# Optimization experiments

Measured on AMD Instinct MI355X. Metric: run time of the kernel, lower is better.

The kernel has to match this reference:

```python
import jax, jax.numpy as jnp
import numpy as np
import math

B, T = 16, 512
P = 256          # num_memory_positions
E = 128          # embedding_dim
NB = 4           # num_beings
K = 4            # attention_radius
TEMP = 8.0       # attention_temperature
PHI = 1.618033988749895


def setup_inputs() -> dict:
    key = jax.random.key(0)
    ks = jax.random.split(key, 8)
    x = jax.random.normal(ks[0], (B, T, 8), jnp.float32)
    W_in = jax.random.normal(ks[1], (8, E), jnp.float32) * 0.1
    b_in = jnp.zeros((E,), jnp.float32)
    W_out = jax.random.normal(ks[2], (E, 8), jnp.float32) * 0.1
    b_out = jnp.zeros((8,), jnp.float32)
    W_p = jax.random.normal(ks[3], (E, E), jnp.float32) * (1.0 / np.sqrt(E))
    b_p = jnp.zeros((E,), jnp.float32)
    ptr_dest = jax.random.uniform(ks[4], (NB, P), jnp.float32) * P
    jump_W = jax.random.normal(ks[5], (NB, E), jnp.float32) * 0.1
    jump_b = jnp.zeros((NB,), jnp.float32)
    ctx_strength = jnp.full((NB,), 0.2, jnp.float32)
    pe = np.zeros((NB, E), np.float32)
    for i in range(NB):
        ph = i * PHI
        v = []
        for h in range(1, 9):
            v += [math.sin(h * ph), math.cos(h * ph)]
        pe[i, :16] = v  # phase_embedding padded with zeros to E (E >= 16)
    phase_bias = jnp.asarray(pe)
    seg = P / NB
    pointer_init = jax.random.uniform(ks[6], (NB, B), jnp.float32) * seg + jnp.arange(NB, dtype=jnp.float32)[:, None] * seg
    return dict(x=x, W_in=W_in, b_in=b_in, W_out=W_out, b_out=b_out,
                W_p=W_p, b_p=b_p, ptr_dest=ptr_dest, jump_W=jump_W,
                jump_b=jump_b, ctx_strength=ctx_strength,
                phase_bias=phase_bias, pointer_init=pointer_init)


def _forward(x, W_in, b_in, W_out, b_out, W_p, b_p, ptr_dest, jump_W,
             jump_b, ctx_strength, phase_bias, pointer_init):
    offsets = jnp.arange(-K, K + 1)          # [W]
    b_ix = jnp.arange(B)                     # [B]
    half = P / 2.0
    ring0 = jnp.zeros((B, P, E), x.dtype)
    hid0 = jnp.zeros((NB, B, E), x.dtype)

    def step(carry, x_t):
        ring, ptrs, hids = carry
        inp = x_t @ W_in + b_in              # [B,E]
        outs, new_ptrs, new_hids = [], [], []
        for i in range(NB):                  # beings sequential (share ring)
            ptr, hid = ptrs[i], hids[i]
            base = jnp.clip(jnp.floor(ptr).astype(jnp.int32), 0, P - 1)
            idx = (base[:, None] + offsets[None, :]) % P            # [B,W]
            delta = jnp.mod(idx.astype(x_t.dtype) - ptr[:, None] + half, P) - half
            w = jax.nn.softmax(-(delta ** 2) / TEMP, axis=1)         # [B,W]
            nbhd = ring[b_ix[:, None], idx]                          # [B,W,E]
            ctx = jnp.sum(w[..., None] * nbhd, axis=1)               # [B,E]
            comb = inp + jax.nn.sigmoid(ctx_strength[i]) * ctx + 0.1 * phase_bias[i]
            s = jnp.tanh(comb + hid)
            s = jnp.tanh(s @ W_p + b_p)      # depth-1 = 1 processing layer
            ring = ring.at[b_ix[:, None], idx].add(w[..., None] * s[:, None, :])
            cur = jnp.clip(ptr.astype(jnp.int32), 0, P - 1)
            jump_target = ptr_dest[i][cur]                           # [B]
            probs = jax.nn.sigmoid(s @ jump_W[i] + jump_b[i])        # [B]
            hard = (probs > 0.5).astype(s.dtype)
            should_jump = hard - jax.lax.stop_gradient(probs) + probs
            walk = (ptr + 1.0) % P
            new_ptrs.append(jnp.where(should_jump > 0.5, jump_target, walk))
            new_hids.append(s)
            outs.append(s @ W_out + b_out)                           # [B,8]
        out_t = jnp.mean(jnp.stack(outs), axis=0)                    # [B,8] (training-mode mean)
        return (ring, jnp.stack(new_ptrs), jnp.stack(new_hids)), out_t

    _, ys = jax.lax.scan(step, (ring0, pointer_init, hid0), jnp.swapaxes(x, 0, 1))
    return jnp.swapaxes(ys, 0, 1)            # [B,T,8]


def reference(x, W_in, b_in, W_out, b_out, W_p, b_p, ptr_dest, jump_W,
              jump_b, ctx_strength, phase_bias, pointer_init):
    return _forward(x, W_in, b_in, W_out, b_out, W_p, b_p, ptr_dest,
                    jump_W, jump_b, ctx_strength, phase_bias, pointer_init)
```

## Files before the change

kernel.cpp:

```cpp
#include <hip/hip_runtime.h>
#include <cmath>

namespace {
constexpr int B_ = 16, T_ = 512, P_ = 256, E_ = 128, NB_ = 4, K_ = 4;
constexpr int THREADS_ = 512;
constexpr int RS_ = 132;

__device__ __forceinline__ float rcpf(float x) { return __builtin_amdgcn_rcpf(x); }
__device__ __forceinline__ float fast_tanh(float x) {
    float a = fabsf(x);
    float t = __expf(-2.0f * a);
    float r = 1.0f - 2.0f * t * rcpf(1.0f + t);
    return copysignf(r, x);
}

__device__ __forceinline__ void lgkm_barrier() {
    __builtin_amdgcn_sched_barrier(0);
    asm volatile("s_waitcnt lgkmcnt(0)\n\ts_barrier" ::: "memory");
    __builtin_amdgcn_sched_barrier(0);
}

template<int CTRL>
__device__ __forceinline__ float dpp_addf(float v) {
    const int s = __builtin_amdgcn_update_dpp(0, __float_as_int(v), CTRL, 0xF, 0xF, true);
    return v + __int_as_float(s);
}
template<int Q>
__device__ __forceinline__ float dpp_bcast4(float v) {
    const int s = __builtin_amdgcn_update_dpp(0, __float_as_int(v), Q * 0x55, 0xF, 0xF, true);
    return __int_as_float(s);
}
template<int Q>
__device__ __forceinline__ int dpp_bcast4i(int v) {
    return __builtin_amdgcn_update_dpp(0, v, Q * 0x55, 0xF, 0xF, true);
}
__device__ __forceinline__ float pl16_sum(float v) {
#if __has_builtin(__builtin_amdgcn_permlane16_swap)
    const unsigned u = __float_as_uint(v);
    const auto r = __builtin_amdgcn_permlane16_swap(u, u, false, false);
    return __uint_as_float(r[0]) + __uint_as_float(r[1]);
#else
    return v + __shfl_xor(v, 16);
#endif
}
__device__ __forceinline__ float pl32_sum(float v) {
#if __has_builtin(__builtin_amdgcn_permlane32_swap)
    const unsigned u = __float_as_uint(v);
    const auto r = __builtin_amdgcn_permlane32_swap(u, u, false, false);
    return __uint_as_float(r[0]) + __uint_as_float(r[1]);
#else
    return v + __shfl_xor(v, 32);
#endif
}
__device__ __forceinline__ float redkq8(float v) {
    v = dpp_addf<0x128>(v);
    v = pl16_sum(v);
    v = pl32_sum(v);
    return v;
}
__device__ __forceinline__ float redpair(float v) {
    v = dpp_addf<0xB1>(v);
    v = dpp_addf<0x4E>(v);
    v = dpp_addf<0x141>(v);
    return v;
}
__device__ __forceinline__ float sel4(int q, float a, float b, float c, float d) {
    const float t0 = (q & 1) ? b : a;
    const float t1 = (q & 1) ? d : c;
    return (q & 2) ? t1 : t0;
}
__device__ __forceinline__ float sel8f(int kq, float w0, float w1, float w2, float w3,
                                       float w4, float w5, float w6, float w7) {
    const float a = (kq & 1) ? w1 : w0;
    const float b = (kq & 1) ? w3 : w2;
    const float c = (kq & 1) ? w5 : w4;
    const float d = (kq & 1) ? w7 : w6;
    const float e = (kq & 2) ? b : a;
    const float f = (kq & 2) ? d : c;
    return (kq & 4) ? f : e;
}
}

__global__ __launch_bounds__(512, 1)
void swarm_ring_kernel(const float* __restrict__ x,
                       const float* __restrict__ W_in,
                       const float* __restrict__ b_in,
                       const float* __restrict__ W_out,
                       const float* __restrict__ b_out,
                       const float* __restrict__ W_p,
                       const float* __restrict__ b_p,
                       const float* __restrict__ ptr_dest,
                       const float* __restrict__ jump_W,
                       const float* __restrict__ jump_b,
                       const float* __restrict__ ctx_strength,
                       const float* __restrict__ phase_bias,
                       const float* __restrict__ pointer_init,
                       float* __restrict__ out)
{
    __shared__ alignas(16) float  ring[P_ * RS_];
    __shared__ alignas(16) float4 s4[136];
    __shared__ alignas(16) float  sbuf[2][160];
    __shared__ alignas(16) float  red[32];
    __shared__ alignas(16) float  hist[16][132];
    __shared__ alignas(16) float  wout_s[8][132];

    const int tid = threadIdx.x;
    const int b   = blockIdx.x;
    const int w   = tid >> 6;
    const int l   = tid & 63;
    const int s_  = l & 7;
    const int kq  = l >> 3;
    const int e0  = ((w << 3) | s_) << 1;
    const int bq  = l & 3;

    for (int k4 = tid; k4 < P_ * RS_ / 4; k4 += THREADS_)
        ((float4*)ring)[k4] = make_float4(0.f, 0.f, 0.f, 0.f);
    for (int idx = tid; idx < 8 * E_; idx += THREADS_) {
        const int m = idx >> 7, ee = idx & 127;
        wout_s[m][ee] = W_out[ee * 8 + m] * 0.25f;
    }

    float2 wp2[16];
    #pragma unroll
    for (int kk = 0; kk < 16; ++kk)
        wp2[kk] = *(const float2*)(W_p + (kq * 16 + kk) * E_ + e0);

    float2 wi2[8];
    #pragma unroll
    for (int k = 0; k < 8; ++k)
        wi2[k] = *(const float2*)(W_in + k * E_ + e0);

    const float2 bin2 = *(const float2*)(b_in + e0);
    const float2 bp2  = *(const float2*)(b_p + e0);
    const float  bout_m = b_out[tid & 7];

    float2 pb2[NB_], jw2[NB_], hid2[NB_];
    float  sigc[NB_], jb_r[NB_], ptrv[NB_];
    #pragma unroll
    for (int i = 0; i < NB_; ++i) {
        const float2 pb = *(const float2*)(phase_bias + i * E_ + e0);
        pb2[i] = make_float2(0.1f * pb.x, 0.1f * pb.y);
        jw2[i] = *(const float2*)(jump_W + i * E_ + e0);
        sigc[i] = 1.0f / (1.0f + __expf(-ctx_strength[i]));
        jb_r[i] = jump_b[i];
        hid2[i] = make_float2(0.f, 0.f);
        ptrv[i] = pointer_init[i * B_ + b];
    }

    const float* xb = x + (size_t)b * T_ * 8;
    float xt[8];
    {
        float4 a0 = ((const float4*)xb)[0], a1 = ((const float4*)xb)[1];
        xt[0]=a0.x; xt[1]=a0.y; xt[2]=a0.z; xt[3]=a0.w;
        xt[4]=a1.x; xt[5]=a1.y; xt[6]=a1.z; xt[7]=a1.w;
    }

    const float Cw1 = 0.8824969f, Cw2 = 0.60653066f, Cw3 = 0.32465247f, Cw4 = 0.13533528f;
    const float Dw1 = 0.7788008f, Dw2 = 0.36787944f, Dw3 = 0.105399225f, Dw4 = 0.018315639f;

    __syncthreads();

    for (int t = 0; t < T_; ++t) {
        const float p_own    = sel4(bq, ptrv[0], ptrv[1], ptrv[2], ptrv[3]);
        const int   base_own = (int)p_own;
        const float jt_own   = ptr_dest[(bq << 8) + base_own];
        const float f_own    = p_own - (float)base_own;
        float wsel_own, w8_own, psinv_own;
        {
            const float r  = __expf(0.25f * f_own);
            const float r2 = r * r, r3 = r2 * r, r4 = r2 * r2;
            const float ri = rcpf(r), ri2 = ri * ri, ri3 = ri2 * ri, ri4 = ri2 * ri2;
            const float p0 = Cw4*ri4, p1 = Cw3*ri3, p2 = Cw2*ri2, p3 = Cw1*ri, p4c = 1.0f,
                        p5 = Cw1*r,  p6 = Cw2*r2,  p7 = Cw3*r3,  p8 = Cw4*r4;
            const float sum = ((p0+p1)+(p2+p3)) + ((p4c+p5)+(p6+p7)) + p8;
            const float inv = rcpf(sum);
            psinv_own = inv;
            wsel_own = sel8f(kq, p0, p1, p2, p3, p4c, p5, p6, p7) * inv;
            w8_own   = p8 * inv;
        }
        int   baseA[NB_];
        float jt[NB_], ws[NB_], w8[NB_];
        baseA[0] = dpp_bcast4i<0>(base_own); baseA[1] = dpp_bcast4i<1>(base_own);
        baseA[2] = dpp_bcast4i<2>(base_own); baseA[3] = dpp_bcast4i<3>(base_own);
        jt[0] = dpp_bcast4<0>(jt_own); jt[1] = dpp_bcast4<1>(jt_own);
        jt[2] = dpp_bcast4<2>(jt_own); jt[3] = dpp_bcast4<3>(jt_own);
        ws[0] = dpp_bcast4<0>(wsel_own); ws[1] = dpp_bcast4<1>(wsel_own);
        ws[2] = dpp_bcast4<2>(wsel_own); ws[3] = dpp_bcast4<3>(wsel_own);
        w8[0] = dpp_bcast4<0>(w8_own); w8[1] = dpp_bcast4<1>(w8_own);
        w8[2] = dpp_bcast4<2>(w8_own); w8[3] = dpp_bcast4<3>(w8_own);

        int ddm[NB_][NB_];
        bool overlap = false;
        #pragma unroll
        for (int j = 1; j < NB_; ++j)
            #pragma unroll
            for (int i = 0; i < j; ++i) {
                const int dd = ((baseA[j] - baseA[i] + 128) & 255) - 128;
                ddm[j][i] = dd;
                overlap = overlap || (dd >= -8 && dd <= 8);
            }

        float2 ctxp2[NB_];
        #pragma unroll
        for (int i = 0; i < NB_; ++i) {
            const int r0 = (baseA[i] + kq - K_) & (P_ - 1);
            const float2 g0 = *(const float2*)(ring + r0 * RS_ + e0);
            float cx = ws[i] * g0.x;
            float cy = ws[i] * g0.y;
            if (kq == 0) {
                const int r2 = (baseA[i] + K_) & (P_ - 1);
                const float2 g2 = *(const float2*)(ring + r2 * RS_ + e0);
                cx = fmaf(w8[i], g2.x, cx);
                cy = fmaf(w8[i], g2.y, cy);
            }
            ctxp2[i] = make_float2(redkq8(cx), redkq8(cy));
        }

        float2 inp2 = bin2;
        #pragma unroll
        for (int k = 0; k < 8; ++k) {
            inp2.x = fmaf(xt[k], wi2[k].x, inp2.x);
            inp2.y = fmaf(xt[k], wi2[k].y, inp2.y);
        }

        float xtn[8];
        if (t + 1 < T_) {
            float4 a0 = ((const float4*)(xb + (t + 1) * 8))[0];
            float4 a1 = ((const float4*)(xb + (t + 1) * 8))[1];
            xtn[0]=a0.x; xtn[1]=a0.y; xtn[2]=a0.z; xtn[3]=a0.w;
            xtn[4]=a1.x; xtn[5]=a1.y; xtn[6]=a1.z; xtn[7]=a1.w;
        } else {
            #pragma unroll
            for (int k = 0; k < 8; ++k) xtn[k] = 0.f;
        }

        float2 sv2[NB_];

        if (!overlap) {
            float2 s1v[NB_];
            #pragma unroll
            for (int j = 0; j < NB_; ++j) {
                s1v[j].x = fast_tanh(fmaf(sigc[j], ctxp2[j].x, inp2.x + pb2[j].x + hid2[j].x));
                s1v[j].y = fast_tanh(fmaf(sigc[j], ctxp2[j].y, inp2.y + pb2[j].y + hid2[j].y));
            }
            if (kq == 0) {
                const int si = 17 * w + (s_ << 1);
                s4[si]     = make_float4(s1v[0].x, s1v[1].x, s1v[2].x, s1v[3].x);
                s4[si + 1] = make_float4(s1v[0].y, s1v[1].y, s1v[2].y, s1v[3].y);
            }
            lgkm_barrier();

            float2 ab0 = make_float2(0.f, 0.f), ab1 = ab0, ab2 = ab0, ab3 = ab0;
            const float4* sp = s4 + kq * 17;
            #pragma unroll
            for (int kk = 0; kk < 16; ++kk) {
                const float4 sq = sp[kk];
                const float2 w2 = wp2[kk];
                ab0.x = fmaf(sq.x, w2.x, ab0.x); ab0.y = fmaf(sq.x, w2.y, ab0.y);
                ab1.x = fmaf(sq.y, w2.x, ab1.x); ab1.y = fmaf(sq.y, w2.y, ab1.y);
                ab2.x = fmaf(sq.z, w2.x, ab2.x); ab2.y = fmaf(sq.z, w2.y, ab2.y);
                ab3.x = fmaf(sq.w, w2.x, ab3.x); ab3.y = fmaf(sq.w, w2.y, ab3.y);
            }
            sv2[0] = make_float2(fast_tanh(redkq8(ab0.x) + bp2.x), fast_tanh(redkq8(ab0.y) + bp2.y));
            sv2[1] = make_float2(fast_tanh(redkq8(ab1.x) + bp2.x), fast_tanh(redkq8(ab1.y) + bp2.y));
            sv2[2] = make_float2(fast_tanh(redkq8(ab2.x) + bp2.x), fast_tanh(redkq8(ab2.y) + bp2.y));
            sv2[3] = make_float2(fast_tanh(redkq8(ab3.x) + bp2.x), fast_tanh(redkq8(ab3.y) + bp2.y));
            #pragma unroll
            for (int j = 0; j < NB_; ++j) hid2[j] = sv2[j];

            #pragma unroll
            for (int j = 0; j < NB_; ++j) {
                const float2 s = sv2[j];
                const int r0 = (baseA[j] + kq - K_) & (P_ - 1);
                float2* q0 = (float2*)(ring + r0 * RS_ + e0);
                float2 v0 = *q0;
                v0.x = fmaf(ws[j], s.x, v0.x); v0.y = fmaf(ws[j], s.y, v0.y);
                *q0 = v0;
                if (kq == 0) {
                    const int r2 = (baseA[j] + K_) & (P_ - 1);
                    float2* q2 = (float2*)(ring + r2 * RS_ + e0);
                    float2 v2 = *q2;
                    v2.x = fmaf(w8[j], s.x, v2.x); v2.y = fmaf(w8[j], s.y, v2.y);
                    *q2 = v2;
                }
            }
        } else {
            float fA[NB_], psinv[NB_];
            fA[0] = dpp_bcast4<0>(f_own); fA[1] = dpp_bcast4<1>(f_own);
            fA[2] = dpp_bcast4<2>(f_own); fA[3] = dpp_bcast4<3>(f_own);
            psinv[0] = dpp_bcast4<0>(psinv_own); psinv[1] = dpp_bcast4<1>(psinv_own);
            psinv[2] = dpp_bcast4<2>(psinv_own); psinv[3] = dpp_bcast4<3>(psinv_own);

            float coefm[NB_][NB_];
            #pragma unroll
            for (int j = 1; j < NB_; ++j) {
                #pragma unroll
                for (int i = 0; i < j; ++i) {
                    const int dd = ddm[j][i];
                    float c = 0.f;
                    if (dd >= -8 && dd <= 8) {
                        const float A = (float)dd - fA[i];
                        const float s  = __expf(-0.25f * (A - fA[j]));
                        const float G  = __expf(0.125f * (fA[i] * fA[i] - A * A));
                        const float s2p = s * s, s3p = s2p * s, s4p = s2p * s2p;
                        const float si = rcpf(s), si2 = si * si, si3 = si2 * si, si4 = si2 * si2;
                        float acc = 0.f;
                        acc += (dd >= 0)              ? Dw4 * si4 : 0.f;
                        acc += (dd >= -1 && dd <= 7)  ? Dw3 * si3 : 0.f;
                        acc += (dd >= -2 && dd <= 6)  ? Dw2 * si2 : 0.f;
                        acc += (dd >= -3 && dd <= 5)  ? Dw1 * si  : 0.f;
                        acc += (dd >= -4 && dd <= 4)  ? 1.0f      : 0.f;
                        acc += (dd >= -5 && dd <= 3)  ? Dw1 * s   : 0.f;
                        acc += (dd >= -6 && dd <= 2)  ? Dw2 * s2p : 0.f;
                        acc += (dd >= -7 && dd <= 1)  ? Dw3 * s3p : 0.f;
                        acc += (dd <= 0)              ? Dw4 * s4p : 0.f;
                        c = psinv[i] * psinv[j] * G * acc;
                    }
                    coefm[j][i] = c;
                }
            }

            #pragma unroll
            for (int j = 0; j < NB_; ++j) {
                float2 ctx = ctxp2[j];
                #pragma unroll
                for (int i = 0; i < j; ++i) {
                    ctx.x = fmaf(coefm[j][i], sv2[i].x, ctx.x);
                    ctx.y = fmaf(coefm[j][i], sv2[i].y, ctx.y);
                }
                float2 s1;
                s1.x = fast_tanh(fmaf(sigc[j], ctx.x, inp2.x + pb2[j].x + hid2[j].x));
                s1.y = fast_tanh(fmaf(sigc[j], ctx.y, inp2.y + pb2[j].y + hid2[j].y));
                if (kq == 0) {
                    const int pf = 20 * w + (s_ << 1);
                    *(float2*)(&sbuf[j & 1][pf]) = s1;
                }
                lgkm_barrier();

                const float4* sp4 = (const float4*)(&sbuf[j & 1][0]);
                float ax = 0.f, ay = 0.f;
                #pragma unroll
                for (int m = 0; m < 4; ++m) {
                    const float4 sq = sp4[5 * kq + m];
                    const float2 wa = wp2[4*m+0], wb = wp2[4*m+1];
                    const float2 wc = wp2[4*m+2], wd = wp2[4*m+3];
                    ax = fmaf(sq.x, wa.x, ax); ay = fmaf(sq.x, wa.y, ay);
                    ax = fmaf(sq.y, wb.x, ax); ay = fmaf(sq.y, wb.y, ay);
                    ax = fmaf(sq.z, wc.x, ax); ay = fmaf(sq.z, wc.y, ay);
                    ax = fmaf(sq.w, wd.x, ax); ay = fmaf(sq.w, wd.y, ay);
                }
                float2 s2;
                s2.x = fast_tanh(redkq8(ax) + bp2.x);
                s2.y = fast_tanh(redkq8(ay) + bp2.y);
                sv2[j] = s2; hid2[j] = s2;

                const int r0 = (baseA[j] + kq - K_) & (P_ - 1);
                float2* q0 = (float2*)(ring + r0 * RS_ + e0);
                float2 v0 = *q0;
                v0.x = fmaf(ws[j], s2.x, v0.x); v0.y = fmaf(ws[j], s2.y, v0.y);
                *q0 = v0;
                if (kq == 0) {
                    const int r2 = (baseA[j] + K_) & (P_ - 1);
                    float2* q2 = (float2*)(ring + r2 * RS_ + e0);
                    float2 v2 = *q2;
                    v2.x = fmaf(w8[j], s2.x, v2.x); v2.y = fmaf(w8[j], s2.y, v2.y);
                    *q2 = v2;
                }
            }
        }

        {
            float vj0 = fmaf(sv2[0].y, jw2[0].y, sv2[0].x * jw2[0].x);
            float vj1 = fmaf(sv2[1].y, jw2[1].y, sv2[1].x * jw2[1].x);
            float vj2 = fmaf(sv2[2].y, jw2[2].y, sv2[2].x * jw2[2].x);
            float vj3 = fmaf(sv2[3].y, jw2[3].y, sv2[3].x * jw2[3].x);
            vj0 = redpair(vj0); vj1 = redpair(vj1); vj2 = redpair(vj2); vj3 = redpair(vj3);
            if (l == 0)
                ((float4*)red)[w] = make_float4(vj0, vj1, vj2, vj3);
        }

        {
            float2 ssum2;
            ssum2.x = (sv2[0].x + sv2[1].x) + (sv2[2].x + sv2[3].x);
            ssum2.y = (sv2[0].y + sv2[1].y) + (sv2[2].y + sv2[3].y);
            if (kq == 0) *(float2*)(&hist[t & 15][e0]) = ssum2;
        }

        lgkm_barrier();

        {
            float rv = red[l & 31];
            rv = dpp_addf<0x124>(rv);
            rv = dpp_addf<0x128>(rv);
            rv = pl16_sum(rv);
            const float zz0 = dpp_bcast4<0>(rv) + jb_r[0];
            const float zz1 = dpp_bcast4<1>(rv) + jb_r[1];
            const float zz2 = dpp_bcast4<2>(rv) + jb_r[2];
            const float zz3 = dpp_bcast4<3>(rv) + jb_r[3];
            const float zz[4] = { zz0, zz1, zz2, zz3 };
            #pragma unroll
            for (int i = 0; i < NB_; ++i) {
                float np;
                if (zz[i] > 0.0f) np = jt[i];
                else { np = ptrv[i] + 1.0f; if (np >= 256.0f) np -= 256.0f; }
                ptrv[i] = np;
            }
        }

        if ((t & 7) == 7 && tid < 64) {
            const int tt = tid >> 3;
            const int m  = tid & 7;
            const float* hrow = hist[(t - 7 + tt) & 15];
            const float* wrow = wout_s[m];
            float acc = 0.f;
            #pragma unroll
            for (int q = 0; q < 32; ++q) {
                const float4 h4 = ((const float4*)hrow)[q];
                const float4 w4 = ((const float4*)wrow)[q];
                acc += ((h4.x * w4.x + h4.y * w4.y) + (h4.z * w4.z + h4.w * w4.w));
            }
            out[((size_t)b * T_ + (t - 7 + tt)) * 8 + m] = acc + bout_m;
        }

        #pragma unroll
        for (int k = 0; k < 8; ++k) xt[k] = xtn[k];
    }
}

extern "C" void kernel_launch(void* const* d_in, const int* in_sizes, int n_in,
                              void* d_out, int out_size, void* d_ws, size_t ws_size,
                              hipStream_t stream) {
    (void)in_sizes; (void)n_in; (void)out_size; (void)d_ws; (void)ws_size;
    swarm_ring_kernel<<<dim3(B_), dim3(THREADS_), 0, stream>>>(
        (const float*)d_in[0],  (const float*)d_in[1],  (const float*)d_in[2],
        (const float*)d_in[3],  (const float*)d_in[4],  (const float*)d_in[5],
        (const float*)d_in[6],  (const float*)d_in[7],  (const float*)d_in[8],
        (const float*)d_in[9],  (const float*)d_in[10], (const float*)d_in[11],
        (const float*)d_in[12], (float*)d_out);
}
```

Before: 1.928 ms.

## Use packed float2 FMAs and spread output projection across all waves

Rewrites the per-element float2 arithmetic with ext_vector_type(2) and elementwise fma, so the compiler can emit packed FP32 instructions (v_pk_fma_f32) on CDNA. It also splits the every-8-step output projection from one wave doing 32-iteration dot products into all 8 waves each doing a 4-iteration partial, followed by an 8-lane reduction. The aim is to shorten the serial per-timestep critical path. The packed ops may add register shuffles, and the redpair reduction must cover exactly 8 lanes for the output to stay correct.

```diff
diff --git a/kernel.cpp b/kernel.cpp
--- a/kernel.cpp
+++ b/kernel.cpp
@@ -5,6 +5,12 @@
 constexpr int B_ = 16, T_ = 512, P_ = 256, E_ = 128, NB_ = 4, K_ = 4;
 constexpr int THREADS_ = 512;
 constexpr int RS_ = 132;
+
+typedef float v2f __attribute__((ext_vector_type(2)));
+__device__ __forceinline__ v2f v2s(float s) { return (v2f){s, s}; }
+__device__ __forceinline__ v2f vfma(v2f a, v2f b, v2f c) {
+    return __builtin_elementwise_fma(a, b, c);
+}
 
 __device__ __forceinline__ float rcpf(float x) { return __builtin_amdgcn_rcpf(x); }
 __device__ __forceinline__ float fast_tanh(float x) {
@@ -120,30 +126,30 @@
         wout_s[m][ee] = W_out[ee * 8 + m] * 0.25f;
     }
 
-    float2 wp2[16];
+    v2f wp2[16];
     #pragma unroll
     for (int kk = 0; kk < 16; ++kk)
-        wp2[kk] = *(const float2*)(W_p + (kq * 16 + kk) * E_ + e0);
-
-    float2 wi2[8];
+        wp2[kk] = *(const v2f*)(W_p + (kq * 16 + kk) * E_ + e0);
+
+    v2f wi2[8];
     #pragma unroll
     for (int k = 0; k < 8; ++k)
-        wi2[k] = *(const float2*)(W_in + k * E_ + e0);
-
-    const float2 bin2 = *(const float2*)(b_in + e0);
-    const float2 bp2  = *(const float2*)(b_p + e0);
-    const float  bout_m = b_out[tid & 7];
-
-    float2 pb2[NB_], jw2[NB_], hid2[NB_];
-    float  sigc[NB_], jb_r[NB_], ptrv[NB_];
+        wi2[k] = *(const v2f*)(W_in + k * E_ + e0);
+
+    const v2f bin2 = *(const v2f*)(b_in + e0);
+    const v2f bp2  = *(const v2f*)(b_p + e0);
+    const float bout_m = b_out[tid & 7];
+
+    v2f   pb2[NB_], jw2[NB_], hid2[NB_];
+    float sigc[NB_], jb_r[NB_], ptrv[NB_];
     #pragma unroll
     for (int i = 0; i < NB_; ++i) {
-        const float2 pb = *(const float2*)(phase_bias + i * E_ + e0);
-        pb2[i] = make_float2(0.1f * pb.x, 0.1f * pb.y);
-        jw2[i] = *(const float2*)(jump_W + i * E_ + e0);
+        const v2f pb = *(const v2f*)(phase_bias + i * E_ + e0);
+        pb2[i] = 0.1f * pb;
+        jw2[i] = *(const v2f*)(jump_W + i * E_ + e0);
         sigc[i] = 1.0f / (1.0f + __expf(-ctx_strength[i]));
         jb_r[i] = jump_b[i];
-        hid2[i] = make_float2(0.f, 0.f);
+        hid2[i] = (v2f){0.f, 0.f};
         ptrv[i] = pointer_init[i * B_ + b];
     }
 
@@ -200,28 +206,24 @@
                 overlap = overlap || (dd >= -8 && dd <= 8);
             }
 
-        float2 ctxp2[NB_];
+        v2f ctxp2[NB_];
         #pragma unroll
         for (int i = 0; i < NB_; ++i) {
             const int r0 = (baseA[i] + kq - K_) & (P_ - 1);
-            const float2 g0 = *(const float2*)(ring + r0 * RS_ + e0);
-            float cx = ws[i] * g0.x;
-            float cy = ws[i] * g0.y;
+            const v2f g0 = *(const v2f*)(ring + r0 * RS_ + e0);
+            v2f c = v2s(ws[i]) * g0;
             if (kq == 0) {
                 const int r2 = (baseA[i] + K_) & (P_ - 1);
-                const float2 g2 = *(const float2*)(ring + r2 * RS_ + e0);
-                cx = fmaf(w8[i], g2.x, cx);
-                cy = fmaf(w8[i], g2.y, cy);
-            }
-            ctxp2[i] = make_float2(redkq8(cx), redkq8(cy));
-        }
-
-        float2 inp2 = bin2;
+                const v2f g2 = *(const v2f*)(ring + r2 * RS_ + e0);
+                c = vfma(v2s(w8[i]), g2, c);
+            }
+            ctxp2[i] = (v2f){redkq8(c[0]), redkq8(c[1])};
+        }
+
+        v2f inp2 = bin2;
         #pragma unroll
-        for (int k = 0; k < 8; ++k) {
-            inp2.x = fmaf(xt[k], wi2[k].x, inp2.x);
-            inp2.y = fmaf(xt[k], wi2[k].y, inp2.y);
-        }
+        for (int k = 0; k < 8; ++k)
+            inp2 = vfma(v2s(xt[k]), wi2[k], inp2);
 
         float xtn[8];
         if (t + 1 < T_) {
@@ -234,54 +236,51 @@
             for (int k = 0; k < 8; ++k) xtn[k] = 0.f;
         }
 
-        float2 sv2[NB_];
+        v2f sv2[NB_];
 
         if (!overlap) {
-            float2 s1v[NB_];
+            v2f s1v[NB_];
             #pragma unroll
             for (int j = 0; j < NB_; ++j) {
-                s1v[j].x = fast_tanh(fmaf(sigc[j], ctxp2[j].x, inp2.x + pb2[j].x + hid2[j].x));
-                s1v[j].y = fast_tanh(fmaf(sigc[j], ctxp2[j].y, inp2.y + pb2[j].y + hid2[j].y));
+                const v2f pre = (inp2 + pb2[j]) + hid2[j];
+                const v2f z   = vfma(v2s(sigc[j]), ctxp2[j], pre);
+                s1v[j] = (v2f){fast_tanh(z[0]), fast_tanh(z[1])};
             }
             if (kq == 0) {
                 const int si = 17 * w + (s_ << 1);
-                s4[si]     = make_float4(s1v[0].x, s1v[1].x, s1v[2].x, s1v[3].x);
-                s4[si + 1] = make_float4(s1v[0].y, s1v[1].y, s1v[2].y, s1v[3].y);
+                s4[si]     = make_float4(s1v[0][0], s1v[1][0], s1v[2][0], s1v[3][0]);
+                s4[si + 1] = make_float4(s1v[0][1], s1v[1][1], s1v[2][1], s1v[3][1]);
             }
             lgkm_barrier();
 
-            float2 ab0 = make_float2(0.f, 0.f), ab1 = ab0, ab2 = ab0, ab3 = ab0;
+            v2f ab0 = (v2f){0.f, 0.f}, ab1 = ab0, ab2 = ab0, ab3 = ab0;
             const float4* sp = s4 + kq * 17;
             #pragma unroll
             for (int kk = 0; kk < 16; ++kk) {
                 const float4 sq = sp[kk];
-                const float2 w2 = wp2[kk];
-                ab0.x = fmaf(sq.x, w2.x, ab0.x); ab0.y = fmaf(sq.x, w2.y, ab0.y);
-                ab1.x = fmaf(sq.y, w2.x, ab1.x); ab1.y = fmaf(sq.y, w2.y, ab1.y);
-                ab2.x = fmaf(sq.z, w2.x, ab2.x); ab2.y = fmaf(sq.z, w2.y, ab2.y);
-                ab3.x = fmaf(sq.w, w2.x, ab3.x); ab3.y = fmaf(sq.w, w2.y, ab3.y);
-            }
-            sv2[0] = make_float2(fast_tanh(redkq8(ab0.x) + bp2.x), fast_tanh(redkq8(ab0.y) + bp2.y));
-            sv2[1] = make_float2(fast_tanh(redkq8(ab1.x) + bp2.x), fast_tanh(redkq8(ab1.y) + bp2.y));
-            sv2[2] = make_float2(fast_tanh(redkq8(ab2.x) + bp2.x), fast_tanh(redkq8(ab2.y) + bp2.y));
-            sv2[3] = make_float2(fast_tanh(redkq8(ab3.x) + bp2.x), fast_tanh(redkq8(ab3.y) + bp2.y));
+                const v2f w2 = wp2[kk];
+                ab0 = vfma(v2s(sq.x), w2, ab0);
+                ab1 = vfma(v2s(sq.y), w2, ab1);
+                ab2 = vfma(v2s(sq.z), w2, ab2);
+                ab3 = vfma(v2s(sq.w), w2, ab3);
+            }
+            sv2[0] = (v2f){fast_tanh(redkq8(ab0[0]) + bp2[0]), fast_tanh(redkq8(ab0[1]) + bp2[1])};
+            sv2[1] = (v2f){fast_tanh(redkq8(ab1[0]) + bp2[0]), fast_tanh(redkq8(ab1[1]) + bp2[1])};
+            sv2[2] = (v2f){fast_tanh(redkq8(ab2[0]) + bp2[0]), fast_tanh(redkq8(ab2[1]) + bp2[1])};
+            sv2[3] = (v2f){fast_tanh(redkq8(ab3[0]) + bp2[0]), fast_tanh(redkq8(ab3[1]) + bp2[1])};
             #pragma unroll
             for (int j = 0; j < NB_; ++j) hid2[j] = sv2[j];
 
             #pragma unroll
             for (int j = 0; j < NB_; ++j) {
-                const float2 s = sv2[j];
+                const v2f s = sv2[j];
                 const int r0 = (baseA[j] + kq - K_) & (P_ - 1);
-                float2* q0 = (float2*)(ring + r0 * RS_ + e0);
-                float2 v0 = *q0;
-                v0.x = fmaf(ws[j], s.x, v0.x); v0.y = fmaf(ws[j], s.y, v0.y);
-                *q0 = v0;
+                v2f* q0 = (v2f*)(ring + r0 * RS_ + e0);
+                *q0 = vfma(v2s(ws[j]), s, *q0);
                 if (kq == 0) {
                     const int r2 = (baseA[j] + K_) & (P_ - 1);
-                    float2* q2 = (float2*)(ring + r2 * RS_ + e0);
-                    float2 v2 = *q2;
-                    v2.x = fmaf(w8[j], s.x, v2.x); v2.y = fmaf(w8[j], s.y, v2.y);
-                    *q2 = v2;
+                    v2f* q2 = (v2f*)(ring + r2 * RS_ + e0);
+                    *q2 = vfma(v2s(w8[j]), s, *q2);
                 }
             }
         } else {
@@ -322,68 +321,58 @@
 
             #pragma unroll
             for (int j = 0; j < NB_; ++j) {
-                float2 ctx = ctxp2[j];
+                v2f ctx = ctxp2[j];
                 #pragma unroll
-                for (int i = 0; i < j; ++i) {
-                    ctx.x = fmaf(coefm[j][i], sv2[i].x, ctx.x);
-                    ctx.y = fmaf(coefm[j][i], sv2[i].y, ctx.y);
-                }
-                float2 s1;
-                s1.x = fast_tanh(fmaf(sigc[j], ctx.x, inp2.x + pb2[j].x + hid2[j].x));
-                s1.y = fast_tanh(fmaf(sigc[j], ctx.y, inp2.y + pb2[j].y + hid2[j].y));
+                for (int i = 0; i < j; ++i)
+                    ctx = vfma(v2s(coefm[j][i]), sv2[i], ctx);
+                const v2f pre = (inp2 + pb2[j]) + hid2[j];
+                const v2f z   = vfma(v2s(sigc[j]), ctx, pre);
+                const v2f s1  = (v2f){fast_tanh(z[0]), fast_tanh(z[1])};
                 if (kq == 0) {
                     const int pf = 20 * w + (s_ << 1);
-                    *(float2*)(&sbuf[j & 1][pf]) = s1;
+                    *(v2f*)(&sbuf[j & 1][pf]) = s1;
                 }
                 lgkm_barrier();
 
                 const float4* sp4 = (const float4*)(&sbuf[j & 1][0]);
-                float ax = 0.f, ay = 0.f;
+                v2f axy = (v2f){0.f, 0.f};
                 #pragma unroll
                 for (int m = 0; m < 4; ++m) {
                     const float4 sq = sp4[5 * kq + m];
-                    const float2 wa = wp2[4*m+0], wb = wp2[4*m+1];
-                    const float2 wc = wp2[4*m+2], wd = wp2[4*m+3];
-                    ax = fmaf(sq.x, wa.x, ax); ay = fmaf(sq.x, wa.y, ay);
-                    ax = fmaf(sq.y, wb.x, ax); ay = fmaf(sq.y, wb.y, ay);
-                    ax = fmaf(sq.z, wc.x, ax); ay = fmaf(sq.z, wc.y, ay);
-                    ax = fmaf(sq.w, wd.x, ax); ay = fmaf(sq.w, wd.y, ay);
+                    axy = vfma(v2s(sq.x), wp2[4*m+0], axy);
+                    axy = vfma(v2s(sq.y), wp2[4*m+1], axy);
+                    axy = vfma(v2s(sq.z), wp2[4*m+2], axy);
+                    axy = vfma(v2s(sq.w), wp2[4*m+3], axy);
                 }
-                float2 s2;
-                s2.x = fast_tanh(redkq8(ax) + bp2.x);
-                s2.y = fast_tanh(redkq8(ay) + bp2.y);
+                v2f s2;
+                s2[0] = fast_tanh(redkq8(axy[0]) + bp2[0]);
+                s2[1] = fast_tanh(redkq8(axy[1]) + bp2[1]);
                 sv2[j] = s2; hid2[j] = s2;
 
                 const int r0 = (baseA[j] + kq - K_) & (P_ - 1);
-                float2* q0 = (float2*)(ring + r0 * RS_ + e0);
-                float2 v0 = *q0;
-                v0.x = fmaf(ws[j], s2.x, v0.x); v0.y = fmaf(ws[j], s2.y, v0.y);
-                *q0 = v0;
+                v2f* q0 = (v2f*)(ring + r0 * RS_ + e0);
+                *q0 = vfma(v2s(ws[j]), s2, *q0);
                 if (kq == 0) {
                     const int r2 = (baseA[j] + K_) & (P_ - 1);
-                    float2* q2 = (float2*)(ring + r2 * RS_ + e0);
-                    float2 v2 = *q2;
-                    v2.x = fmaf(w8[j], s2.x, v2.x); v2.y = fmaf(w8[j], s2.y, v2.y);
-                    *q2 = v2;
+                    v2f* q2 = (v2f*)(ring + r2 * RS_ + e0);
+                    *q2 = vfma(v2s(w8[j]), s2, *q2);
                 }
             }
         }
 
         {
-            float vj0 = fmaf(sv2[0].y, jw2[0].y, sv2[0].x * jw2[0].x);
-            float vj1 = fmaf(sv2[1].y, jw2[1].y, sv2[1].x * jw2[1].x);
-            float vj2 = fmaf(sv2[2].y, jw2[2].y, sv2[2].x * jw2[2].x);
-            float vj3 = fmaf(sv2[3].y, jw2[3].y, sv2[3].x * jw2[3].x);
+            float vj0 = fmaf(sv2[0][1], jw2[0][1], sv2[0][0] * jw2[0][0]);
+            float vj1 = fmaf(sv2[1][1], jw2[1][1], sv2[1][0] * jw2[1][0]);
+            float vj2 = fmaf(sv2[2][1], jw2[2][1], sv2[2][0] * jw2[2][0]);
+            float vj3 = fmaf(sv2[3][1], jw2[3][1], sv2[3][0] * jw2[3][0]);
             vj0 = redpair(vj0); vj1 = redpair(vj1); vj2 = redpair(vj2); vj3 = redpair(vj3);
             if (l == 0)
                 ((float4*)red)[w] = make_float4(vj0, vj1, vj2, vj3);
         }
 
         {
-            float2 ssum2;
-            ssum2.x = (sv2[0].x + sv2[1].x) + (sv2[2].x + sv2[3].x);
-            ssum2.y = (sv2[0].y + sv2[1].y) + (sv2[2].y + sv2[3].y);
-            if (kq == 0) *(float2*)(&hist[t & 15][e0]) = ssum2;
+            const v2f ssum2 = (sv2[0] + sv2[1]) + (sv2[2] + sv2[3]);
+            if (kq == 0) *(v2f*)(&hist[t & 15][e0]) = ssum2;
         }
 
         lgkm_barrier();
@@ -407,19 +396,22 @@
             }
         }
 
-        if ((t & 7) == 7 && tid < 64) {
-            const int tt = tid >> 3;
-            const int m  = tid & 7;
+        if ((t & 7) == 7) {
+            const int tt = w;
+            const int m  = l >> 3;
+            const int c4 = l & 7;
             const float* hrow = hist[(t - 7 + tt) & 15];
             const float* wrow = wout_s[m];
             float acc = 0.f;
             #pragma unroll
-            for (int q = 0; q < 32; ++q) {
-                const float4 h4 = ((const float4*)hrow)[q];
-                const float4 w4 = ((const float4*)wrow)[q];
+            for (int q = 0; q < 4; ++q) {
+                const float4 h4 = ((const float4*)hrow)[c4 * 4 + q];
+                const float4 w4 = ((const float4*)wrow)[c4 * 4 + q];
                 acc += ((h4.x * w4.x + h4.y * w4.y) + (h4.z * w4.z + h4.w * w4.w));
             }
-            out[((size_t)b * T_ + (t - 7 + tt)) * 8 + m] = acc + bout_m;
+            acc = redpair(acc);
+            if ((l & 7) == 0)
+                out[((size_t)b * T_ + (t - 7 + tt)) * 8 + m] = acc + bout_m;
         }
 
         #pragma unroll
@@ -431,7 +423,7 @@
                               void* d_out, int out_size, void* d_ws, size_t ws_size,
                               hipStream_t stream) {
     (void)in_sizes; (void)n_in; (void)out_size; (void)d_ws; (void)ws_size;
-    swarm_ring_kernel<<<dim3(B_), dim3(THREADS_), 0, stream>>>(
+    swarm_ring_kernel<<<dim3(B_), dim3(512), 0, stream>>>(
         (const float*)d_in[0],  (const float*)d_in[1],  (const float*)d_in[2],
         (const float*)d_in[3],  (const float*)d_in[4],  (const float*)d_in[5],
         (const float*)d_in[6],  (const float*)d_in[7],  (const float*)d_in[8],
```

Result: no change. 1.902 ms (-1.4%).
